# Performance work log

Measured on AMD Instinct MI355X. Metric: run time of the kernel, lower is better.

Reference implementation:

```python
import jax, jax.numpy as jnp
import numpy as np

B, S, D = 2, 2048, 2048
H = 16
HD = D // H  # 128

def setup_inputs() -> dict:
    key = jax.random.key(0)
    k1, k2, k3 = jax.random.split(key, 3)
    x = jax.random.normal(k1, (B, S, D), dtype=jnp.float32)
    w_qkv = jax.random.normal(k2, (D, 3 * D), dtype=jnp.float32) * (1.0 / np.sqrt(D))
    b_qkv = jnp.zeros((3 * D,), dtype=jnp.float32)
    w_out = jax.random.normal(k3, (D, D), dtype=jnp.float32) * (1.0 / np.sqrt(D))
    b_out = jnp.zeros((D,), dtype=jnp.float32)
    return {"x": x, "w_qkv": w_qkv, "b_qkv": b_qkv, "w_out": w_out, "b_out": b_out}

def reference(x, w_qkv, b_qkv, w_out, b_out):
    batch, seq_len, channels = x.shape
    qkv = x @ w_qkv + b_qkv                      # [B,S,3D]
    q, k, v = jnp.split(qkv, 3, axis=-1)
    # [B,S,D] -> [B,H,S,HD]
    def heads(t):
        return t.reshape(batch, seq_len, H, HD).transpose(0, 2, 1, 3)
    q, k, v = heads(q), heads(k), heads(v)
    scale = 1.0 / np.sqrt(HD).astype(np.float32)
    attn = jnp.einsum('bhqd,bhkd->bhqk', q, k) * scale
    causal = jnp.tril(jnp.ones((seq_len, seq_len), dtype=bool))
    attn = jnp.where(causal, attn, -jnp.inf)
    attn = jax.nn.softmax(attn, axis=-1)
    y = jnp.einsum('bhqk,bhkd->bhqd', attn, v)   # [B,H,S,HD]
    y = y.transpose(0, 2, 1, 3).reshape(batch, seq_len, channels)
    return y @ w_out + b_out
```

## Files before the change

### kernel.cpp

```cpp
#include <hip/hip_runtime.h>
#include <hip/hip_bf16.h>
#include <cstdint>
#include <cstddef>

#define BB 2
#define SS 2048
#define DD 2048
#define HH 16
#define HDIM 128
#define QSCALE 0.12751743f

typedef short bf16x8 __attribute__((ext_vector_type(8)));
typedef float f32x4 __attribute__((ext_vector_type(4)));
typedef float f32x16 __attribute__((ext_vector_type(16)));

__device__ __forceinline__ ushort f2bf(float f) {
    union { float f; uint32_t u; } v; v.f = f;
    uint32_t u = v.u;
    u += 0x7fffu + ((u >> 16) & 1u);
    return (ushort)(u >> 16);
}

__device__ __forceinline__ ushort f2bf_fast(float f) {
    union { float f; uint32_t u; } v; v.f = f;
    return (ushort)((v.u + 0x8000u) >> 16);
}

__device__ __forceinline__ void gl16(const ushort* g, ushort* l) {
    __builtin_amdgcn_global_load_lds(
        (const __attribute__((address_space(1))) unsigned int*)g,
        (__attribute__((address_space(3))) unsigned int*)l,
        16, 0, 0);
}

__global__ __launch_bounds__(256) void cast_x_kernel(
    const float* __restrict__ X, ushort* __restrict__ Xb)
{
    size_t idx = ((size_t)blockIdx.x * 256 + threadIdx.x) * 8;
    float4 a = *(const float4*)(X + idx);
    float4 b = *(const float4*)(X + idx + 4);
    ushort4 o0, o1;
    o0.x = f2bf(a.x); o0.y = f2bf(a.y); o0.z = f2bf(a.z); o0.w = f2bf(a.w);
    o1.x = f2bf(b.x); o1.y = f2bf(b.y); o1.z = f2bf(b.z); o1.w = f2bf(b.w);
    *(ushort4*)(Xb + idx) = o0;
    *(ushort4*)(Xb + idx + 4) = o1;
}

__global__ __launch_bounds__(256) void transpose_cast_kernel(
    const float* __restrict__ W, ushort* __restrict__ Wt, int K, int N)
{
    __shared__ ushort tile[32][36];
    const int n0 = blockIdx.x * 32;
    const int k0 = blockIdx.y * 32;
    const int t = threadIdx.x;
    const int r = t >> 3;
    const int c = (t & 7) * 4;
    float4 a = *(const float4*)(W + (size_t)(k0 + r) * N + n0 + c);
    tile[r][c + 0] = f2bf(a.x); tile[r][c + 1] = f2bf(a.y);
    tile[r][c + 2] = f2bf(a.z); tile[r][c + 3] = f2bf(a.w);
    __syncthreads();
    ushort4 o;
    o.x = tile[c + 0][r]; o.y = tile[c + 1][r];
    o.z = tile[c + 2][r]; o.w = tile[c + 3][r];
    *(ushort4*)(Wt + (size_t)(n0 + r) * K + k0 + c) = o;
}

__global__ __launch_bounds__(256) void transpose_v_kernel(
    const ushort* __restrict__ V, ushort* __restrict__ Vt)
{
    __shared__ ushort tile[32][36];
    const int s0 = blockIdx.x * 32;
    const int h0 = blockIdx.y * 32;
    const int bh = blockIdx.z;
    const ushort* Vp = V + (size_t)bh * SS * HDIM;
    ushort* Vtp = Vt + (size_t)bh * HDIM * SS;
    const int t = threadIdx.x;
    const int r = t >> 3;
    const int c = (t & 7) * 4;
    *(ushort4*)&tile[r][c] = *(const ushort4*)(Vp + (size_t)(s0 + r) * HDIM + h0 + c);
    __syncthreads();
    ushort4 o;
    o.x = tile[c + 0][r]; o.y = tile[c + 1][r];
    o.z = tile[c + 2][r]; o.w = tile[c + 3][r];
    *(ushort4*)(Vtp + (size_t)(h0 + r) * SS + s0 + c) = o;
}

__global__ __launch_bounds__(256) void gemm_qkv_kernel(
    const ushort* __restrict__ A, const ushort* __restrict__ Bt,
    const float* __restrict__ bias,
    ushort* __restrict__ Qo, ushort* __restrict__ Ko, ushort* __restrict__ Vo)
{
    const int n0 = blockIdx.x * 128;
    const int m0 = blockIdx.y * 128;
    __shared__ ushort As[128 * 32];
    __shared__ ushort Bs[128 * 32];
    const int t = threadIdx.x, w = t >> 6, lane = t & 63;
    const int l31 = lane & 31, hh = lane >> 5;
    const int lrow = lane >> 2, lks = lane & 3;
    const int wr = w >> 1, wc = w & 1;
    const int swst = (lrow >> 1) & 3;
    const int swr  = (l31 >> 1) & 3;

    f32x16 acc[2][2];
#pragma unroll
    for (int i = 0; i < 2; ++i)
#pragma unroll
        for (int j = 0; j < 2; ++j) acc[i][j] = (f32x16)0.f;

    for (int k0 = 0; k0 < DD; k0 += 32) {
        __syncthreads();
#pragma unroll
        for (int q = 0; q < 2; ++q) {
            int e = w * 2 + q;
            int row = e * 16 + lrow;
            gl16(A  + (size_t)(m0 + row) * DD + k0 + (lks ^ swst) * 8, &As[e * 512]);
            gl16(Bt + (size_t)(n0 + row) * DD + k0 + (lks ^ swst) * 8, &Bs[e * 512]);
        }
        __syncthreads();
#pragma unroll
        for (int k16 = 0; k16 < 2; ++k16) {
            int co = ((k16 * 2 + hh) ^ swr) * 8;
            bf16x8 ar0 = *(const bf16x8*)&As[(wr * 64 + l31) * 32 + co];
            bf16x8 ar1 = *(const bf16x8*)&As[(wr * 64 + 32 + l31) * 32 + co];
            bf16x8 br0 = *(const bf16x8*)&Bs[(wc * 64 + l31) * 32 + co];
            bf16x8 br1 = *(const bf16x8*)&Bs[(wc * 64 + 32 + l31) * 32 + co];
            acc[0][0] = __builtin_amdgcn_mfma_f32_32x32x16_bf16(ar0, br0, acc[0][0], 0, 0, 0);
            acc[0][1] = __builtin_amdgcn_mfma_f32_32x32x16_bf16(ar0, br1, acc[0][1], 0, 0, 0);
            acc[1][0] = __builtin_amdgcn_mfma_f32_32x32x16_bf16(ar1, br0, acc[1][0], 0, 0, 0);
            acc[1][1] = __builtin_amdgcn_mfma_f32_32x32x16_bf16(ar1, br1, acc[1][1], 0, 0, 0);
        }
    }

    const int bidx = m0 >> 11;
    const int which = n0 >> 11;
    ushort* dst = (which == 0) ? Qo : ((which == 1) ? Ko : Vo);
    const float sc = (which == 0) ? QSCALE : 1.0f;
#pragma unroll
    for (int j = 0; j < 2; ++j) {
        int n = n0 + wc * 64 + j * 32 + l31;
        int c = n & 2047, h = c >> 7, hd = c & 127;
        float bv = bias[n];
        size_t base = ((size_t)(bidx * HH + h) * SS) * HDIM + hd;
#pragma unroll
        for (int i = 0; i < 2; ++i) {
#pragma unroll
            for (int r = 0; r < 16; ++r) {
                int s = (m0 & 2047) + wr * 64 + i * 32 + (r & 3) + 8 * (r >> 2) + 4 * hh;
                dst[base + (size_t)s * HDIM] = f2bf((acc[i][j][r] + bv) * sc);
            }
        }
    }
}

__global__ __launch_bounds__(256) void gemm_out_kernel(
    const ushort* __restrict__ A, const ushort* __restrict__ Bt,
    const float* __restrict__ bias, float* __restrict__ Out)
{
    const int n0 = blockIdx.x * 128;
    const int m0 = blockIdx.y * 128;
    __shared__ ushort As[128 * 32];
    __shared__ ushort Bs[128 * 32];
    const int t = threadIdx.x, w = t >> 6, lane = t & 63;
    const int l31 = lane & 31, hh = lane >> 5;
    const int lrow = lane >> 2, lks = lane & 3;
    const int wr = w >> 1, wc = w & 1;
    const int swst = (lrow >> 1) & 3;
    const int swr  = (l31 >> 1) & 3;

    f32x16 acc[2][2];
#pragma unroll
    for (int i = 0; i < 2; ++i)
#pragma unroll
        for (int j = 0; j < 2; ++j) acc[i][j] = (f32x16)0.f;

    for (int k0 = 0; k0 < DD; k0 += 32) {
        __syncthreads();
#pragma unroll
        for (int q = 0; q < 2; ++q) {
            int e = w * 2 + q;
            int row = e * 16 + lrow;
            gl16(A  + (size_t)(m0 + row) * DD + k0 + (lks ^ swst) * 8, &As[e * 512]);
            gl16(Bt + (size_t)(n0 + row) * DD + k0 + (lks ^ swst) * 8, &Bs[e * 512]);
        }
        __syncthreads();
#pragma unroll
        for (int k16 = 0; k16 < 2; ++k16) {
            int co = ((k16 * 2 + hh) ^ swr) * 8;
            bf16x8 ar0 = *(const bf16x8*)&As[(wr * 64 + l31) * 32 + co];
            bf16x8 ar1 = *(const bf16x8*)&As[(wr * 64 + 32 + l31) * 32 + co];
            bf16x8 br0 = *(const bf16x8*)&Bs[(wc * 64 + l31) * 32 + co];
            bf16x8 br1 = *(const bf16x8*)&Bs[(wc * 64 + 32 + l31) * 32 + co];
            acc[0][0] = __builtin_amdgcn_mfma_f32_32x32x16_bf16(ar0, br0, acc[0][0], 0, 0, 0);
            acc[0][1] = __builtin_amdgcn_mfma_f32_32x32x16_bf16(ar0, br1, acc[0][1], 0, 0, 0);
            acc[1][0] = __builtin_amdgcn_mfma_f32_32x32x16_bf16(ar1, br0, acc[1][0], 0, 0, 0);
            acc[1][1] = __builtin_amdgcn_mfma_f32_32x32x16_bf16(ar1, br1, acc[1][1], 0, 0, 0);
        }
    }

#pragma unroll
    for (int j = 0; j < 2; ++j) {
        int n = n0 + wc * 64 + j * 32 + l31;
        float bv = bias[n];
#pragma unroll
        for (int i = 0; i < 2; ++i) {
#pragma unroll
            for (int r = 0; r < 16; ++r) {
                int m = m0 + wr * 64 + i * 32 + (r & 3) + 8 * (r >> 2) + 4 * hh;
                Out[(size_t)m * DD + n] = acc[i][j][r] + bv;
            }
        }
    }
}

__global__ __launch_bounds__(256, 2) void attn_mfma_kernel(
    const ushort* __restrict__ Q, const ushort* __restrict__ K,
    const ushort* __restrict__ Vt, ushort* __restrict__ Y)
{
    const int bh = blockIdx.y;
    const int qt = gridDim.x - 1 - blockIdx.x;
    const int q0 = qt * 128;
    const int b = bh >> 4, h = bh & 15;

    __shared__ ushort Ks[2][4 * 64 * 32];
    __shared__ ushort Vs[2][2 * 128 * 32];
    __shared__ ushort Ps[128 * 32];

    const int t = threadIdx.x, w = t >> 6, lane = t & 63;
    const int l31 = lane & 31, hh = lane >> 5;
    const int lrow = lane >> 2, lks = lane & 3;
    const int swst = (lrow >> 1) & 3;
    const int swr  = (l31 >> 1) & 3;

    const ushort* Qp = Q  + (size_t)bh * SS * HDIM;
    const ushort* Kp = K  + (size_t)bh * SS * HDIM;
    const ushort* Vp = Vt + (size_t)bh * HDIM * SS;

    bf16x8 aq[8];
#pragma unroll
    for (int kb2 = 0; kb2 < 8; ++kb2)
        aq[kb2] = *(const bf16x8*)(Qp + (size_t)(q0 + w * 32 + l31) * HDIM + kb2 * 16 + hh * 8);

    bf16x8 ones;
#pragma unroll
    for (int j = 0; j < 8; ++j) ones[j] = (short)0x3F80;

    f32x16 O[4];
#pragma unroll
    for (int nt = 0; nt < 4; ++nt) O[nt] = (f32x16)0.f;
    f32x16 Ol = (f32x16)0.f;

    const int kbdiag = 2 * qt + (w >> 1);
    const int nkb = 2 * qt + 2;

#define STAGE_KV(kb_, s_) do {                                                  \
    const int kbase_ = (kb_) * 64;                                              \
    _Pragma("unroll")                                                           \
    for (int g = 0; g < 4; ++g) {                                               \
        int key = g * 16 + lrow;                                                \
        gl16(Kp + (size_t)(kbase_ + key) * HDIM + w * 32 + (lks ^ swst) * 8,    \
             &Ks[s_][w * 2048 + g * 512]);                                      \
    }                                                                           \
    _Pragma("unroll")                                                           \
    for (int g = 0; g < 4; ++g) {                                               \
        int pan = g >> 1, sub = g & 1;                                          \
        int dim = w * 32 + sub * 16 + lrow;                                     \
        gl16(Vp + (size_t)dim * SS + kbase_ + pan * 32 + (lks ^ swst) * 8,      \
             &Vs[s_][pan * 4096 + (w * 32 + sub * 16) * 32]);                   \
    }                                                                           \
} while (0)

    STAGE_KV(0, 0);

    for (int kb = 0; kb < nkb; ++kb) {
        const int kbase = kb * 64;
        const int slot = kb & 1;

        if (kb + 1 < nkb) {
            STAGE_KV(kb + 1, slot ^ 1);
            asm volatile("s_waitcnt vmcnt(8)" ::: "memory");
        } else {
            asm volatile("s_waitcnt vmcnt(0)" ::: "memory");
        }
        __builtin_amdgcn_s_barrier();

        const ushort* KsS = Ks[slot];
        const ushort* VsS = Vs[slot];

        if (kb <= kbdiag) {
            f32x16 sc0 = (f32x16)0.f, sc1 = (f32x16)0.f;
            __builtin_amdgcn_s_setprio(1);
#pragma unroll
            for (int kb2 = 0; kb2 < 8; ++kb2) {
                int co = (((kb2 & 1) * 2 + hh) ^ swr) * 8;
                bf16x8 bk0 = *(const bf16x8*)&KsS[(kb2 >> 1) * 2048 + l31 * 32 + co];
                bf16x8 bk1 = *(const bf16x8*)&KsS[(kb2 >> 1) * 2048 + (32 + l31) * 32 + co];
                sc0 = __builtin_amdgcn_mfma_f32_32x32x16_bf16(aq[kb2], bk0, sc0, 0, 0, 0);
                sc1 = __builtin_amdgcn_mfma_f32_32x32x16_bf16(aq[kb2], bk1, sc1, 0, 0, 0);
            }
            __builtin_amdgcn_s_setprio(0);

            if (kb == kbdiag) {
#pragma unroll
                for (int r = 0; r < 16; ++r) {
                    int rowg = q0 + w * 32 + (r & 3) + 8 * (r >> 2) + 4 * hh;
                    if (kbase + l31 > rowg)      sc0[r] = -1e30f;
                    if (kbase + 32 + l31 > rowg) sc1[r] = -1e30f;
                }
            }

#pragma unroll
            for (int half = 0; half < 2; ++half) {
#pragma unroll
                for (int r = 0; r < 16; ++r) {
                    float sv = (half == 0) ? sc0[r] : sc1[r];
                    float p = __builtin_amdgcn_exp2f(sv);
                    int rowm = (r & 3) + 8 * (r >> 2) + 4 * hh;
                    int pc = (l31 >> 3) ^ ((rowm >> 1) & 3);
                    Ps[(w * 32 + rowm) * 32 + (pc << 3) + (l31 & 7)] = f2bf_fast(p);
                }
                __builtin_amdgcn_s_setprio(1);
#pragma unroll
                for (int kblk2 = 0; kblk2 < 2; ++kblk2) {
                    int co = ((kblk2 * 2 + hh) ^ swr) * 8;
                    bf16x8 ap = *(const bf16x8*)&Ps[(w * 32 + l31) * 32 + co];
#pragma unroll
                    for (int nt = 0; nt < 4; ++nt) {
                        bf16x8 bv = *(const bf16x8*)&VsS[half * 4096 + (nt * 32 + l31) * 32 + co];
                        O[nt] = __builtin_amdgcn_mfma_f32_32x32x16_bf16(ap, bv, O[nt], 0, 0, 0);
                    }
                    Ol = __builtin_amdgcn_mfma_f32_32x32x16_bf16(ap, ones, Ol, 0, 0, 0);
                }
                __builtin_amdgcn_s_setprio(0);
            }
        }
        __builtin_amdgcn_s_barrier();
    }
#undef STAGE_KV

#pragma unroll
    for (int r = 0; r < 16; ++r) {
        int s = q0 + w * 32 + (r & 3) + 8 * (r >> 2) + 4 * hh;
        float inv = 1.0f / Ol[r];
        size_t base = ((size_t)(b * SS + s)) * DD + h * HDIM;
#pragma unroll
        for (int nt = 0; nt < 4; ++nt)
            Y[base + nt * 32 + l31] = f2bf(O[nt][r] * inv);
    }
}

extern "C" void kernel_launch(void* const* d_in, const int* in_sizes, int n_in,
                              void* d_out, int out_size, void* d_ws, size_t ws_size,
                              hipStream_t stream) {
    const float* x     = (const float*)d_in[0];
    const float* w_qkv = (const float*)d_in[1];
    const float* b_qkv = (const float*)d_in[2];
    const float* w_out = (const float*)d_in[3];
    const float* b_out = (const float*)d_in[4];
    float* out = (float*)d_out;

    ushort* ws  = (ushort*)d_ws;
    ushort* xb  = ws;
    ushort* wtq = xb + 8388608;
    ushort* wto = wtq + 12582912;
    ushort* q   = wto + 4194304;
    ushort* k   = q + 8388608;
    ushort* v   = k + 8388608;
    ushort* vt  = v + 8388608;
    ushort* y   = vt + 8388608;

    cast_x_kernel<<<4096, 256, 0, stream>>>(x, xb);
    transpose_cast_kernel<<<dim3(192, 64), 256, 0, stream>>>(w_qkv, wtq, DD, 3 * DD);
    transpose_cast_kernel<<<dim3(64, 64), 256, 0, stream>>>(w_out, wto, DD, DD);
    gemm_qkv_kernel<<<dim3(48, 32), 256, 0, stream>>>(xb, wtq, b_qkv, q, k, v);
    transpose_v_kernel<<<dim3(64, 4, 32), 256, 0, stream>>>(v, vt);
    attn_mfma_kernel<<<dim3(16, 32), 256, 0, stream>>>(q, k, vt, y);
    gemm_out_kernel<<<dim3(16, 32), 256, 0, stream>>>(y, wto, b_out, out);
}
```

Baseline: 399.6 us.

## Compute transposed scores and pass P to PV MFMA via lane shuffles

The score MFMA operands are swapped so each lane holds scores along keys for a single query row. P can then be packed into bf16 registers and exchanged between half-waves with a cross-lane shuffle, instead of being written to and read back from a shared-memory P buffer. This drops the LDS round trip and the Ps allocation, which lowers LDS traffic and shared-memory footprint. The cost is extra packing and select instructions plus a dependence on the exact MFMA register layout being handled correctly.

```diff
diff --git a/kernel.cpp b/kernel.cpp
--- a/kernel.cpp
+++ b/kernel.cpp
@@ -223,7 +223,6 @@
 
     __shared__ ushort Ks[2][4 * 64 * 32];
     __shared__ ushort Vs[2][2 * 128 * 32];
-    __shared__ ushort Ps[128 * 32];
 
     const int t = threadIdx.x, w = t >> 6, lane = t & 63;
     const int l31 = lane & 31, hh = lane >> 5;
@@ -251,6 +250,8 @@
 
     const int kbdiag = 2 * qt + (w >> 1);
     const int nkb = 2 * qt + 2;
+    const bool hi = (hh == 1);
+    const int qg = q0 + w * 32 + l31;
 
 #define STAGE_KV(kb_, s_) do {                                                  \
     const int kbase_ = (kb_) * 64;                                              \
@@ -287,50 +288,64 @@
         const ushort* VsS = Vs[slot];
 
         if (kb <= kbdiag) {
-            f32x16 sc0 = (f32x16)0.f, sc1 = (f32x16)0.f;
+            f32x16 st0 = (f32x16)0.f, st1 = (f32x16)0.f;
             __builtin_amdgcn_s_setprio(1);
 #pragma unroll
             for (int kb2 = 0; kb2 < 8; ++kb2) {
                 int co = (((kb2 & 1) * 2 + hh) ^ swr) * 8;
                 bf16x8 bk0 = *(const bf16x8*)&KsS[(kb2 >> 1) * 2048 + l31 * 32 + co];
                 bf16x8 bk1 = *(const bf16x8*)&KsS[(kb2 >> 1) * 2048 + (32 + l31) * 32 + co];
-                sc0 = __builtin_amdgcn_mfma_f32_32x32x16_bf16(aq[kb2], bk0, sc0, 0, 0, 0);
-                sc1 = __builtin_amdgcn_mfma_f32_32x32x16_bf16(aq[kb2], bk1, sc1, 0, 0, 0);
+                st0 = __builtin_amdgcn_mfma_f32_32x32x16_bf16(bk0, aq[kb2], st0, 0, 0, 0);
+                st1 = __builtin_amdgcn_mfma_f32_32x32x16_bf16(bk1, aq[kb2], st1, 0, 0, 0);
             }
             __builtin_amdgcn_s_setprio(0);
 
             if (kb == kbdiag) {
 #pragma unroll
                 for (int r = 0; r < 16; ++r) {
-                    int rowg = q0 + w * 32 + (r & 3) + 8 * (r >> 2) + 4 * hh;
-                    if (kbase + l31 > rowg)      sc0[r] = -1e30f;
-                    if (kbase + 32 + l31 > rowg) sc1[r] = -1e30f;
+                    int keyr = kbase + (r & 3) + 8 * (r >> 2) + 4 * hh;
+                    if (keyr > qg)      st0[r] = -1e30f;
+                    if (keyr + 32 > qg) st1[r] = -1e30f;
                 }
             }
 
 #pragma unroll
             for (int half = 0; half < 2; ++half) {
-#pragma unroll
-                for (int r = 0; r < 16; ++r) {
-                    float sv = (half == 0) ? sc0[r] : sc1[r];
-                    float p = __builtin_amdgcn_exp2f(sv);
-                    int rowm = (r & 3) + 8 * (r >> 2) + 4 * hh;
-                    int pc = (l31 >> 3) ^ ((rowm >> 1) & 3);
-                    Ps[(w * 32 + rowm) * 32 + (pc << 3) + (l31 & 7)] = f2bf_fast(p);
+                float p[16];
+#pragma unroll
+                for (int r = 0; r < 16; ++r)
+                    p[r] = __builtin_amdgcn_exp2f((half == 0) ? st0[r] : st1[r]);
+                uint w0[4], w1[4];
+#pragma unroll
+                for (int g = 0; g < 4; ++g) {
+                    w0[g] = (uint)f2bf_fast(p[4 * g])
+                          | ((uint)f2bf_fast(p[4 * g + 1]) << 16);
+                    w1[g] = (uint)f2bf_fast(p[4 * g + 2])
+                          | ((uint)f2bf_fast(p[4 * g + 3]) << 16);
                 }
-                __builtin_amdgcn_s_setprio(1);
 #pragma unroll
                 for (int kblk2 = 0; kblk2 < 2; ++kblk2) {
+                    uint own0 = hi ? w0[2 * kblk2 + 1] : w0[2 * kblk2];
+                    uint own1 = hi ? w1[2 * kblk2 + 1] : w1[2 * kblk2];
+                    uint snd0 = hi ? w0[2 * kblk2]     : w0[2 * kblk2 + 1];
+                    uint snd1 = hi ? w1[2 * kblk2]     : w1[2 * kblk2 + 1];
+                    uint ps0 = (uint)__shfl_xor((int)snd0, 32, 64);
+                    uint ps1 = (uint)__shfl_xor((int)snd1, 32, 64);
+                    union { uint u[4]; bf16x8 v; } fr;
+                    fr.u[0] = hi ? ps0 : own0;
+                    fr.u[1] = hi ? ps1 : own1;
+                    fr.u[2] = hi ? own0 : ps0;
+                    fr.u[3] = hi ? own1 : ps1;
                     int co = ((kblk2 * 2 + hh) ^ swr) * 8;
-                    bf16x8 ap = *(const bf16x8*)&Ps[(w * 32 + l31) * 32 + co];
+                    __builtin_amdgcn_s_setprio(1);
 #pragma unroll
                     for (int nt = 0; nt < 4; ++nt) {
                         bf16x8 bv = *(const bf16x8*)&VsS[half * 4096 + (nt * 32 + l31) * 32 + co];
-                        O[nt] = __builtin_amdgcn_mfma_f32_32x32x16_bf16(ap, bv, O[nt], 0, 0, 0);
+                        O[nt] = __builtin_amdgcn_mfma_f32_32x32x16_bf16(fr.v, bv, O[nt], 0, 0, 0);
                     }
-                    Ol = __builtin_amdgcn_mfma_f32_32x32x16_bf16(ap, ones, Ol, 0, 0, 0);
+                    Ol = __builtin_amdgcn_mfma_f32_32x32x16_bf16(fr.v, ones, Ol, 0, 0, 0);
+                    __builtin_amdgcn_s_setprio(0);
                 }
-                __builtin_amdgcn_s_setprio(0);
             }
         }
         __builtin_amdgcn_s_barrier();
```

Result: no change. 406.4 us (+1.7%).
